# Performance work log

Hardware: AMD Instinct MI355X
Metric: run time of the kernel (lower is better)

Reference implementation:

```python
import math
import jax, jax.numpy as jnp
import numpy as np

D_EMBD = 1024
N_HEAD = 16
BLOCK = 2048
B, T = 4, 2048


def setup_inputs() -> dict:
    key = jax.random.key(0)
    ks = jax.random.split(key, 5)
    d = D_EMBD
    return {
        "x": jax.random.normal(ks[0], (B, T, d), dtype=jnp.float32),
        "Wq": jax.random.normal(ks[1], (d, d), dtype=jnp.float32),
        "bq": jnp.zeros((d,), dtype=jnp.float32),
        "Wk": jax.random.normal(ks[2], (d, d), dtype=jnp.float32),
        "bk": jnp.zeros((d,), dtype=jnp.float32),
        "Wv": jax.random.normal(ks[3], (d, d), dtype=jnp.float32),
        "bv": jnp.zeros((d,), dtype=jnp.float32),
        "Wp": jax.random.normal(ks[4], (d, d), dtype=jnp.float32),
        "bp": jnp.zeros((d,), dtype=jnp.float32),
    }


def reference(x, Wq, bq, Wk, bk, Wv, bv, Wp, bp):
    Bb, Tt, C = x.shape
    n_head = N_HEAD
    hd = C // n_head  # head dim
    # QKV projections -> [B, H, T, hd]
    def split_heads(y):
        return y.reshape(Bb, Tt, n_head, hd).transpose(0, 2, 1, 3)
    Q = split_heads(x @ Wq + bq)
    K = split_heads(x @ Wk + bk)
    V = split_heads(x @ Wv + bv)
    # scores [B, H, T, T]
    attn = jnp.einsum('bhqd,bhkd->bhqk', Q, K) / math.sqrt(hd)
    # causal mask: -inf strictly above diagonal (matches triu(ones*-inf, 1))
    causal = jnp.tril(jnp.ones((Tt, Tt), dtype=bool))
    attn = jnp.where(causal, attn, -jnp.inf)
    attn = jax.nn.softmax(attn, axis=-1)
    y = jnp.einsum('bhqk,bhkd->bhqd', attn, V)
    y = y.transpose(0, 2, 1, 3).reshape(Bb, Tt, C)
    return y @ Wp + bp
```

## Files before the change

kernel.cpp:

```cpp
#include <hip/hip_runtime.h>
#include <stdint.h>
#include <stddef.h>

#define TT 2048
#define CC 1024
#define BBATCH 4
#define HH 16
#define HD 64
#define MTOT (BBATCH * TT)

typedef __bf16 bf16_t;
typedef __bf16 bf16x4 __attribute__((ext_vector_type(4)));
typedef __bf16 bf16x8 __attribute__((ext_vector_type(8)));
typedef float f32x4 __attribute__((ext_vector_type(4)));

typedef const __attribute__((address_space(1))) uint32_t* as1_u32p;
typedef __attribute__((address_space(3))) uint32_t* as3_u32p;

__device__ __forceinline__ f32x4 mfma16(bf16x8 a, bf16x8 b, f32x4 c) {
  return __builtin_amdgcn_mfma_f32_16x16x32_bf16(a, b, c, 0, 0, 0);
}

__device__ __forceinline__ void gload_lds16(void* lds, const void* g) {
  __builtin_amdgcn_global_load_lds((as1_u32p)g, (as3_u32p)lds, 16, 0, 0);
}

__device__ __forceinline__ bf16x8 rd32(const char* t, int row, int lane) {
  int sl = (lane >> 4) ^ ((row >> 1) & 3);
  return *(const bf16x8*)(t + row * 64 + sl * 16);
}
__device__ __forceinline__ bf16x8 rd64(const char* t, int row, int kk, int lane) {
  int sl = ((lane >> 4) + kk * 4) ^ (row & 7);
  return *(const bf16x8*)(t + row * 128 + sl * 16);
}

__global__ void split_x_kernel(const float* __restrict__ x, bf16_t* __restrict__ xh,
                               bf16_t* __restrict__ xl, int n4) {
  int stride = gridDim.x * blockDim.x;
  for (int i = blockIdx.x * blockDim.x + threadIdx.x; i < n4; i += stride) {
    float4 v = ((const float4*)x)[i];
    float vv[4] = {v.x, v.y, v.z, v.w};
    bf16x4 hv, lv;
#pragma unroll
    for (int j = 0; j < 4; ++j) {
      bf16_t h = (bf16_t)vv[j];
      hv[j] = h;
      lv[j] = (bf16_t)(vv[j] - (float)h);
    }
    *(bf16x4*)(xh + (size_t)i * 4) = hv;
    *(bf16x4*)(xl + (size_t)i * 4) = lv;
  }
}

__global__ void transpose_split_kernel(const float* __restrict__ Wq, const float* __restrict__ Wk,
                                       const float* __restrict__ Wv, const float* __restrict__ Wp,
                                       bf16_t* __restrict__ wqkh, bf16_t* __restrict__ wqkl,
                                       bf16_t* __restrict__ wv_t, bf16_t* __restrict__ wp_t) {
  __shared__ float tile[32][33];
  int mat = blockIdx.z;
  const float* W = (mat == 0) ? Wq : (mat == 1) ? Wk : (mat == 2) ? Wv : Wp;
  int tx = threadIdx.x, ty = threadIdx.y;
  int n0 = blockIdx.x * 32, k0 = blockIdx.y * 32;
#pragma unroll
  for (int j = 0; j < 32; j += 8)
    tile[ty + j][tx] = W[(size_t)(k0 + ty + j) * CC + n0 + tx];
  __syncthreads();
#pragma unroll
  for (int j = 0; j < 32; j += 8) {
    float v = tile[tx][ty + j];
    int n = n0 + ty + j, k = k0 + tx;
    if (mat <= 1) {
      bf16_t h = (bf16_t)v;
      size_t o = (size_t)(mat * CC + n) * CC + k;
      wqkh[o] = h;
      wqkl[o] = (bf16_t)(v - (float)h);
    } else {
      bf16_t* dst = (mat == 2) ? wv_t : wp_t;
      dst[(size_t)n * CC + k] = (bf16_t)v;
    }
  }
}

template <int MODE>
__global__ __launch_bounds__(256) void gemm_kernel(
    const bf16_t* __restrict__ Ah, const bf16_t* __restrict__ Al,
    const bf16_t* __restrict__ Bh, const bf16_t* __restrict__ Bl,
    const float* __restrict__ bias0, const float* __restrict__ bias1,
    void* __restrict__ out0, void* __restrict__ out1,
    void* __restrict__ out2, void* __restrict__ out3) {
  constexpr int NT = (MODE == 0) ? 4 : 2;
  __shared__ __align__(16) char smem[NT * 8192];
  char* sAh = smem;
  char* sAl = smem + 8192;
  char* sBh = smem + (MODE == 0 ? 16384 : 8192);
  char* sBl = smem + 24576;

  const int bn = blockIdx.x, bm = blockIdx.y;
  const int tid = threadIdx.x, w = tid >> 6, lane = tid & 63;
  const int wr = w >> 1, wc = w & 1;

  f32x4 acc[4][4] = {};

  for (int ks = 0; ks < 32; ++ks) {
    const int k0 = ks * 32;
    __syncthreads();
#pragma unroll
    for (int it = 0; it < 2; ++it) {
      int c = it * 4 + w;
      int row = c * 16 + (lane >> 2);
      int sl = (lane & 3) ^ ((row >> 1) & 3);
      size_t aoff = (size_t)(bm * 128 + row) * CC + k0 + sl * 8;
      size_t boff = (size_t)(bn * 128 + row) * CC + k0 + sl * 8;
      gload_lds16(sAh + c * 1024, Ah + aoff);
      gload_lds16(sBh + c * 1024, Bh + boff);
      if (MODE == 0) {
        gload_lds16(sAl + c * 1024, Al + aoff);
        gload_lds16(sBl + c * 1024, Bl + boff);
      }
    }
    __syncthreads();

    bf16x8 afh[4], bfh[4], afl[4], bfl[4];
#pragma unroll
    for (int i = 0; i < 4; ++i) {
      int ar = wr * 64 + i * 16 + (lane & 15);
      int br = wc * 64 + i * 16 + (lane & 15);
      afh[i] = rd32(sAh, ar, lane);
      bfh[i] = rd32(sBh, br, lane);
      if (MODE == 0) {
        afl[i] = rd32(sAl, ar, lane);
        bfl[i] = rd32(sBl, br, lane);
      }
    }
#pragma unroll
    for (int mi = 0; mi < 4; ++mi) {
#pragma unroll
      for (int ni = 0; ni < 4; ++ni) {
        acc[mi][ni] = mfma16(afh[mi], bfh[ni], acc[mi][ni]);
        if (MODE == 0) {
          acc[mi][ni] = mfma16(afh[mi], bfl[ni], acc[mi][ni]);
          acc[mi][ni] = mfma16(afl[mi], bfh[ni], acc[mi][ni]);
        }
      }
    }
  }

#pragma unroll
  for (int mi = 0; mi < 4; ++mi) {
#pragma unroll
    for (int ni = 0; ni < 4; ++ni) {
      const int col = bn * 128 + wc * 64 + ni * 16 + (lane & 15);
#pragma unroll
      for (int r = 0; r < 4; ++r) {
        const int row = bm * 128 + wr * 64 + mi * 16 + (lane >> 4) * 4 + r;
        float v = acc[mi][ni][r];
        if (MODE == 0) {
          const int which = col >> 10, c1 = col & 1023;
          const int h = c1 >> 6, d = c1 & 63;
          const int b = row >> 11, t = row & 2047;
          v += which ? bias1[c1] : bias0[c1];
          if (!which) v *= 0.125f;
          const size_t off = ((size_t)(b * HH + h) * TT + t) * HD + d;
          bf16_t hi = (bf16_t)v;
          bf16_t lo = (bf16_t)(v - (float)hi);
          ((bf16_t*)(which ? out2 : out0))[off] = hi;
          ((bf16_t*)(which ? out3 : out1))[off] = lo;
        } else if (MODE == 1) {
          const int h = col >> 6, d = col & 63;
          const int b = row >> 11, t = row & 2047;
          float vv = v + bias0[col];
          ((bf16_t*)out0)[((size_t)(b * HH + h) * HD + d) * TT + t] = (bf16_t)vv;
        } else {
          ((float*)out0)[(size_t)row * CC + col] = v + bias0[col];
        }
      }
    }
  }
}

__global__ __launch_bounds__(512, 4) void attn_kernel(
    const bf16_t* __restrict__ qh, const bf16_t* __restrict__ ql,
    const bf16_t* __restrict__ kh, const bf16_t* __restrict__ kl,
    const bf16_t* __restrict__ vt, bf16_t* __restrict__ y) {
  __shared__ __align__(16) char s_kh[2][8192];
  __shared__ __align__(16) char s_kl[2][8192];
  __shared__ __align__(16) char s_vt[2][8192];
  __shared__ __align__(16) char s_p[8][2048];

  const int blk = blockIdx.x;
  const int bh = blk >> 3;
  const int p = blk & 7;
  const int b = bh >> 4, h = bh & 15;
  const int tid = threadIdx.x, w = tid >> 6, lane = tid & 63;

  const int st_row = w * 8 + (lane >> 3);
  const int st_sl = (lane & 7) ^ (st_row & 7);
  const size_t st_koff0 = ((size_t)bh * TT + st_row) * HD + st_sl * 8;
  const size_t st_voff0 = ((size_t)bh * HD + st_row) * TT + st_sl * 8;

#pragma unroll
  for (int half = 0; half < 2; ++half) {
    const int qb = half ? (15 - p) : p;
    const int ktmax = 2 * qb + 1;
    const int qrow0 = qb * 128 + w * 16;

    bf16x8 qhf[2], qlf[2];
#pragma unroll
    for (int kk = 0; kk < 2; ++kk) {
      size_t off = ((size_t)bh * TT + qrow0 + (lane & 15)) * HD + kk * 32 + (lane >> 4) * 8;
      qhf[kk] = *(const bf16x8*)(qh + off);
      qlf[kk] = *(const bf16x8*)(ql + off);
    }

    f32x4 o[4] = {};
    float m[4], l[4];
#pragma unroll
    for (int r = 0; r < 4; ++r) { m[r] = -1e30f; l[r] = 0.f; }

    gload_lds16(s_kh[0] + w * 1024, kh + st_koff0);
    gload_lds16(s_kl[0] + w * 1024, kl + st_koff0);
    gload_lds16(s_vt[0] + w * 1024, vt + st_voff0);

    int cur = 0;
    for (int kt = 0; kt <= ktmax; ++kt) {
      if (kt < ktmax) {
        const size_t koff = st_koff0 + (size_t)(kt + 1) * 64 * HD;
        const size_t voff = st_voff0 + (size_t)(kt + 1) * 64;
        gload_lds16(s_kh[cur ^ 1] + w * 1024, kh + koff);
        gload_lds16(s_kl[cur ^ 1] + w * 1024, kl + koff);
        gload_lds16(s_vt[cur ^ 1] + w * 1024, vt + voff);
        asm volatile("s_waitcnt vmcnt(3)" ::: "memory");
      } else {
        asm volatile("s_waitcnt vmcnt(0)" ::: "memory");
      }
      __builtin_amdgcn_s_barrier();

      const char* ckh = s_kh[cur];
      const char* ckl = s_kl[cur];
      const char* cvt = s_vt[cur];
      const bool active = (qrow0 + 15 >= kt * 64);
      if (active) {
        float sarr[4][4];
#pragma unroll
        for (int cf = 0; cf < 4; ++cf) {
          f32x4 s = {};
#pragma unroll
          for (int kk = 0; kk < 2; ++kk) {
            bf16x8 kfh = rd64(ckh, cf * 16 + (lane & 15), kk, lane);
            bf16x8 kfl = rd64(ckl, cf * 16 + (lane & 15), kk, lane);
            s = mfma16(qhf[kk], kfh, s);
            s = mfma16(qhf[kk], kfl, s);
            s = mfma16(qlf[kk], kfh, s);
          }
#pragma unroll
          for (int r = 0; r < 4; ++r) sarr[cf][r] = s[r];
        }

        if (kt * 64 + 63 > qrow0) {
#pragma unroll
          for (int cf = 0; cf < 4; ++cf) {
            int kc = kt * 64 + cf * 16 + (lane & 15);
#pragma unroll
            for (int r = 0; r < 4; ++r) {
              int qr = qrow0 + (lane >> 4) * 4 + r;
              if (kc > qr) sarr[cf][r] = -1e30f;
            }
          }
        }

#pragma unroll
        for (int r = 0; r < 4; ++r) {
          float tmax = fmaxf(fmaxf(sarr[0][r], sarr[1][r]), fmaxf(sarr[2][r], sarr[3][r]));
          tmax = fmaxf(tmax, __shfl_xor(tmax, 1));
          tmax = fmaxf(tmax, __shfl_xor(tmax, 2));
          tmax = fmaxf(tmax, __shfl_xor(tmax, 4));
          tmax = fmaxf(tmax, __shfl_xor(tmax, 8));
          float mnew = fmaxf(m[r], tmax);
          float sc = __expf(m[r] - mnew);
          float ps = 0.f;
          const int prow = (lane >> 4) * 4 + r;
#pragma unroll
          for (int cf = 0; cf < 4; ++cf) {
            float pv = __expf(sarr[cf][r] - mnew);
            ps += pv;
            int byt = prow * 128 + (((cf * 16 + (lane & 15)) * 2) ^ ((prow & 7) << 4));
            *(bf16_t*)(&s_p[w][0] + byt) = (bf16_t)pv;
          }
          ps += __shfl_xor(ps, 1);
          ps += __shfl_xor(ps, 2);
          ps += __shfl_xor(ps, 4);
          ps += __shfl_xor(ps, 8);
          l[r] = l[r] * sc + ps;
          m[r] = mnew;
#pragma unroll
          for (int cd = 0; cd < 4; ++cd) o[cd][r] *= sc;
        }

#pragma unroll
        for (int kk = 0; kk < 2; ++kk) {
          bf16x8 pf = rd64(&s_p[w][0], lane & 15, kk, lane);
#pragma unroll
          for (int cd = 0; cd < 4; ++cd) {
            bf16x8 vf = rd64(cvt, cd * 16 + (lane & 15), kk, lane);
            o[cd] = mfma16(pf, vf, o[cd]);
          }
        }
      }

      asm volatile("s_waitcnt lgkmcnt(0)" ::: "memory");
      __builtin_amdgcn_s_barrier();
      cur ^= 1;
    }

#pragma unroll
    for (int cd = 0; cd < 4; ++cd) {
#pragma unroll
      for (int r = 0; r < 4; ++r) {
        int t = qrow0 + (lane >> 4) * 4 + r;
        int col = h * HD + cd * 16 + (lane & 15);
        y[(size_t)(b * TT + t) * CC + col] = (bf16_t)(o[cd][r] / l[r]);
      }
    }
  }
}

extern "C" void kernel_launch(void* const* d_in, const int* in_sizes, int n_in,
                              void* d_out, int out_size, void* d_ws, size_t ws_size,
                              hipStream_t stream) {
  (void)in_sizes; (void)n_in; (void)out_size; (void)ws_size;
  const float* x  = (const float*)d_in[0];
  const float* Wq = (const float*)d_in[1];
  const float* bq = (const float*)d_in[2];
  const float* Wk = (const float*)d_in[3];
  const float* bk = (const float*)d_in[4];
  const float* Wv = (const float*)d_in[5];
  const float* bv = (const float*)d_in[6];
  const float* Wp = (const float*)d_in[7];
  const float* bp = (const float*)d_in[8];

  char* ws = (char*)d_ws;
  const size_t MB = 1024 * 1024;
  bf16_t* xh   = (bf16_t*)(ws + 0 * MB);
  bf16_t* xl   = (bf16_t*)(ws + 16 * MB);
  bf16_t* wqkh = (bf16_t*)(ws + 32 * MB);
  bf16_t* wqkl = (bf16_t*)(ws + 36 * MB);
  bf16_t* wv_t = (bf16_t*)(ws + 40 * MB);
  bf16_t* wp_t = (bf16_t*)(ws + 42 * MB);
  bf16_t* qhw  = (bf16_t*)(ws + 44 * MB);
  bf16_t* qlw  = (bf16_t*)(ws + 60 * MB);
  bf16_t* khw  = (bf16_t*)(ws + 76 * MB);
  bf16_t* klw  = (bf16_t*)(ws + 92 * MB);
  bf16_t* vtw  = (bf16_t*)(ws + 108 * MB);
  bf16_t* yw   = (bf16_t*)(ws + 124 * MB);

  split_x_kernel<<<2048, 256, 0, stream>>>(x, xh, xl, MTOT * CC / 4);
  transpose_split_kernel<<<dim3(32, 32, 4), dim3(32, 8), 0, stream>>>(
      Wq, Wk, Wv, Wp, wqkh, wqkl, wv_t, wp_t);
  gemm_kernel<0><<<dim3(16, 64), 256, 0, stream>>>(
      xh, xl, wqkh, wqkl, bq, bk, qhw, qlw, khw, klw);
  gemm_kernel<1><<<dim3(8, 64), 256, 0, stream>>>(
      xh, nullptr, wv_t, nullptr, bv, nullptr, vtw, nullptr, nullptr, nullptr);
  attn_kernel<<<512, 512, 0, stream>>>(qhw, qlw, khw, klw, vtw, yw);
  gemm_kernel<2><<<dim3(8, 64), 256, 0, stream>>>(
      yw, nullptr, wp_t, nullptr, bp, nullptr, d_out, nullptr, nullptr, nullptr);
}
```

Before: 298.9 us.

## Transpose attention MFMA operands so each lane owns one query row

Swaps the A/B operands of the QK^T and PV MFMAs so the accumulator is transposed and each lane holds a single query row. The softmax max and sum then reduce mostly inside registers, with two cross-lane shuffles instead of four per row, and P is written to LDS as packed bf16x4 vectors instead of scalar bf16 stores. Output stores also become 4-wide vectors. Block-to-(batch,head) mapping is reordered so that consecutive blocks cover different heads for the same query-block pair, which changes load balance and cache locality.

```diff
diff --git a/kernel.cpp b/kernel.cpp
--- a/kernel.cpp
+++ b/kernel.cpp
@@ -188,10 +188,11 @@
   __shared__ __align__(16) char s_p[8][2048];
 
   const int blk = blockIdx.x;
-  const int bh = blk >> 3;
-  const int p = blk & 7;
+  const int bh = (blk & 7) * 8 + ((blk >> 3) & 7);
+  const int p = blk >> 6;
   const int b = bh >> 4, h = bh & 15;
   const int tid = threadIdx.x, w = tid >> 6, lane = tid & 63;
+  const int hi = lane >> 4, qi = lane & 15;
 
   const int st_row = w * 8 + (lane >> 3);
   const int st_sl = (lane & 7) ^ (st_row & 7);
@@ -203,19 +204,18 @@
     const int qb = half ? (15 - p) : p;
     const int ktmax = 2 * qb + 1;
     const int qrow0 = qb * 128 + w * 16;
+    const int qv = qrow0 + qi;
 
     bf16x8 qhf[2], qlf[2];
 #pragma unroll
     for (int kk = 0; kk < 2; ++kk) {
-      size_t off = ((size_t)bh * TT + qrow0 + (lane & 15)) * HD + kk * 32 + (lane >> 4) * 8;
+      size_t off = ((size_t)bh * TT + qrow0 + qi) * HD + kk * 32 + hi * 8;
       qhf[kk] = *(const bf16x8*)(qh + off);
       qlf[kk] = *(const bf16x8*)(ql + off);
     }
 
     f32x4 o[4] = {};
-    float m[4], l[4];
-#pragma unroll
-    for (int r = 0; r < 4; ++r) { m[r] = -1e30f; l[r] = 0.f; }
+    float m = -1e30f, l = 0.f;
 
     gload_lds16(s_kh[0] + w * 1024, kh + st_koff0);
     gload_lds16(s_kl[0] + w * 1024, kl + st_koff0);
@@ -240,69 +240,69 @@
       const char* cvt = s_vt[cur];
       const bool active = (qrow0 + 15 >= kt * 64);
       if (active) {
-        float sarr[4][4];
+        f32x4 st[4];
 #pragma unroll
         for (int cf = 0; cf < 4; ++cf) {
           f32x4 s = {};
 #pragma unroll
           for (int kk = 0; kk < 2; ++kk) {
-            bf16x8 kfh = rd64(ckh, cf * 16 + (lane & 15), kk, lane);
-            bf16x8 kfl = rd64(ckl, cf * 16 + (lane & 15), kk, lane);
-            s = mfma16(qhf[kk], kfh, s);
-            s = mfma16(qhf[kk], kfl, s);
-            s = mfma16(qlf[kk], kfh, s);
+            bf16x8 kfh = rd64(ckh, cf * 16 + qi, kk, lane);
+            bf16x8 kfl = rd64(ckl, cf * 16 + qi, kk, lane);
+            s = mfma16(kfh, qhf[kk], s);
+            s = mfma16(kfl, qhf[kk], s);
+            s = mfma16(kfh, qlf[kk], s);
           }
-#pragma unroll
-          for (int r = 0; r < 4; ++r) sarr[cf][r] = s[r];
+          st[cf] = s;
         }
 
         if (kt * 64 + 63 > qrow0) {
 #pragma unroll
-          for (int cf = 0; cf < 4; ++cf) {
-            int kc = kt * 64 + cf * 16 + (lane & 15);
-#pragma unroll
-            for (int r = 0; r < 4; ++r) {
-              int qr = qrow0 + (lane >> 4) * 4 + r;
-              if (kc > qr) sarr[cf][r] = -1e30f;
-            }
+          for (int cf = 0; cf < 4; ++cf)
+#pragma unroll
+            for (int r = 0; r < 4; ++r)
+              if (kt * 64 + cf * 16 + hi * 4 + r > qv) st[cf][r] = -1e30f;
+        }
+
+        float tmax = st[0][0];
+#pragma unroll
+        for (int cf = 0; cf < 4; ++cf)
+#pragma unroll
+          for (int r = 0; r < 4; ++r) tmax = fmaxf(tmax, st[cf][r]);
+        tmax = fmaxf(tmax, __shfl_xor(tmax, 16));
+        tmax = fmaxf(tmax, __shfl_xor(tmax, 32));
+        const float mnew = fmaxf(m, tmax);
+        const float sc = __expf(m - mnew);
+        float ps = 0.f;
+#pragma unroll
+        for (int cf = 0; cf < 4; ++cf) {
+          bf16x4 pp;
+#pragma unroll
+          for (int r = 0; r < 4; ++r) {
+            float pv = __expf(st[cf][r] - mnew);
+            ps += pv;
+            pp[r] = (bf16_t)pv;
           }
-        }
-
-#pragma unroll
-        for (int r = 0; r < 4; ++r) {
-          float tmax = fmaxf(fmaxf(sarr[0][r], sarr[1][r]), fmaxf(sarr[2][r], sarr[3][r]));
-          tmax = fmaxf(tmax, __shfl_xor(tmax, 1));
-          tmax = fmaxf(tmax, __shfl_xor(tmax, 2));
-          tmax = fmaxf(tmax, __shfl_xor(tmax, 4));
-          tmax = fmaxf(tmax, __shfl_xor(tmax, 8));
-          float mnew = fmaxf(m[r], tmax);
-          float sc = __expf(m[r] - mnew);
-          float ps = 0.f;
-          const int prow = (lane >> 4) * 4 + r;
-#pragma unroll
-          for (int cf = 0; cf < 4; ++cf) {
-            float pv = __expf(sarr[cf][r] - mnew);
-            ps += pv;
-            int byt = prow * 128 + (((cf * 16 + (lane & 15)) * 2) ^ ((prow & 7) << 4));
-            *(bf16_t*)(&s_p[w][0] + byt) = (bf16_t)pv;
-          }
-          ps += __shfl_xor(ps, 1);
-          ps += __shfl_xor(ps, 2);
-          ps += __shfl_xor(ps, 4);
-          ps += __shfl_xor(ps, 8);
-          l[r] = l[r] * sc + ps;
-          m[r] = mnew;
-#pragma unroll
-          for (int cd = 0; cd < 4; ++cd) o[cd][r] *= sc;
+          int slot = ((cf << 1) + (hi >> 1)) ^ qi & 7;
+          slot = ((cf << 1) + (hi >> 1)) ^ (qi & 7);
+          *(bf16x4*)(&s_p[w][0] + qi * 128 + slot * 16 + (hi & 1) * 8) = pp;
+        }
+        ps += __shfl_xor(ps, 16);
+        ps += __shfl_xor(ps, 32);
+        l = l * sc + ps;
+        m = mnew;
+#pragma unroll
+        for (int cd = 0; cd < 4; ++cd) {
+#pragma unroll
+          for (int r = 0; r < 4; ++r) o[cd][r] *= sc;
         }
 
 #pragma unroll
         for (int kk = 0; kk < 2; ++kk) {
-          bf16x8 pf = rd64(&s_p[w][0], lane & 15, kk, lane);
+          bf16x8 pf = rd64(&s_p[w][0], qi, kk, lane);
 #pragma unroll
           for (int cd = 0; cd < 4; ++cd) {
-            bf16x8 vf = rd64(cvt, cd * 16 + (lane & 15), kk, lane);
-            o[cd] = mfma16(pf, vf, o[cd]);
+            bf16x8 vf = rd64(cvt, cd * 16 + qi, kk, lane);
+            o[cd] = mfma16(vf, pf, o[cd]);
           }
         }
       }
@@ -312,14 +312,14 @@
       cur ^= 1;
     }
 
+    const float inv = 1.f / l;
+    const int t = qrow0 + qi;
 #pragma unroll
     for (int cd = 0; cd < 4; ++cd) {
-#pragma unroll
-      for (int r = 0; r < 4; ++r) {
-        int t = qrow0 + (lane >> 4) * 4 + r;
-        int col = h * HD + cd * 16 + (lane & 15);
-        y[(size_t)(b * TT + t) * CC + col] = (bf16_t)(o[cd][r] / l[r]);
-      }
+      bf16x4 ov;
+#pragma unroll
+      for (int r = 0; r < 4; ++r) ov[r] = (bf16_t)(o[cd][r] * inv);
+      *(bf16x4*)(y + (size_t)(b * TT + t) * CC + h * HD + cd * 16 + hi * 4) = ov;
     }
   }
 }
```

Measured after the change: 257.3 us. 13.9% less time.
